# Kernel tuning notes

Hardware: AMD Instinct MI355X
Metric: run time of the kernel (lower is better)

## Reference

```python
import jax, jax.numpy as jnp
import numpy as np

HID = 64   # basis_hidden_dim
NB = 8     # num_learnable_bases
N = 16     # n_super_nodes
D = 4      # latent_dim
B = 2048   # batch

_PNAMES = ["W1", "b1", "W2", "b2", "W3", "b3", "scale", "aW1", "ab1", "aW2", "ab2", "res"]


def _basis_params(key, din):
    ks = jax.random.split(key, 4)
    s = 0.1
    return [
        jax.random.normal(ks[0], (NB, din, HID)) * s, jnp.zeros((NB, HID)),
        jax.random.normal(ks[1], (NB, HID, HID)) * s, jnp.zeros((NB, HID)),
        jax.random.normal(ks[2], (NB, HID, 1)) * s, jnp.zeros((NB, 1)),
        jnp.ones((NB,)),
        jax.random.normal(ks[3], (din, HID // 2)) * s, jnp.zeros((HID // 2,)),
        jax.random.normal(jax.random.fold_in(ks[3], 1), (HID // 2, NB)) * s, jnp.zeros((NB,)),
        jnp.ones((1,)) * 0.1,
    ]


def setup_inputs() -> dict:
    key = jax.random.key(0)
    k0, k1, k2, k3, k4 = jax.random.split(key, 5)
    inp = {"z_flat": jax.random.normal(k0, (B, N * D), dtype=jnp.float32)}
    for pfx, kk, din in [("pw", k1, 8), ("nd", k2, D), ("gl", k3, N * D)]:
        for nm, v in zip(_PNAMES, _basis_params(kk, din)):
            inp[pfx + "_" + nm] = v
    ks = jax.random.split(k4, 3)
    inp["sel_W1"] = jax.random.normal(ks[0], (N * D, HID)) * 0.1
    inp["sel_b1"] = jnp.zeros((HID,))
    inp["sel_W2"] = jax.random.normal(ks[1], (HID, HID // 2)) * 0.1
    inp["sel_b2"] = jnp.zeros((HID // 2,))
    inp["sel_W3"] = jax.random.normal(ks[2], (HID // 2, 1)) * 0.1
    inp["sel_b3"] = jnp.zeros((1,))
    return inp


def _basis(x, W1, b1, W2, b2, W3, b3, scale, aW1, ab1, aW2, ab2, res):
    # x: [..., din] -> [..., 1]. NB tiny 3-layer MLPs batched over basis axis n.
    h = jax.nn.silu(jnp.einsum('...i,nih->...nh', x, W1) + b1)
    h = jax.nn.silu(jnp.einsum('...nh,nhk->...nk', h, W2) + b2)
    o = (jnp.einsum('...nh,nh->...n', h, W3[..., 0]) + b3[:, 0]) * scale  # [..., NB]
    # attention mixing over the NB basis outputs
    a = jax.nn.silu(x @ aW1 + ab1)
    a = jax.nn.softmax(a @ aW2 + ab2, axis=-1)                            # [..., NB]
    out = jnp.sum(o * a, axis=-1, keepdims=True)
    return out + res * jnp.mean(x, axis=-1, keepdims=True)                # residual


def _forward(z_flat,
             pw_W1, pw_b1, pw_W2, pw_b2, pw_W3, pw_b3, pw_scale, pw_aW1, pw_ab1, pw_aW2, pw_ab2, pw_res,
             nd_W1, nd_b1, nd_W2, nd_b2, nd_W3, nd_b3, nd_scale, nd_aW1, nd_ab1, nd_aW2, nd_ab2, nd_res,
             gl_W1, gl_b1, gl_W2, gl_b2, gl_W3, gl_b3, gl_scale, gl_aW1, gl_ab1, gl_aW2, gl_ab2, gl_res,
             sel_W1, sel_b1, sel_W2, sel_b2, sel_W3, sel_b3):
    b = z_flat.shape[0]
    z_nodes = z_flat.reshape(b, N, D)
    pos = z_nodes[:, :, :2]
    iu, ju = jnp.triu_indices(N, k=1)  # P = N*(N-1)/2 = 120 pairs
    # pairwise distances on upper-triangular pairs (no box wrap: box_size=None)
    diffs = pos[:, iu] - pos[:, ju]                     # [B, P, 2]
    d = jnp.sqrt(jnp.sum(diffs * diffs, axis=-1))       # [B, P]
    d = jnp.maximum(d, 0.001)
    inv_d = 1.0 / (d + 0.1)
    inv_sq = 1.0 / (d * d + 0.1)
    exp_d = jnp.exp(-jnp.minimum(d, 20.0))
    screened = exp_d / (d + 0.1)
    log_d = jnp.log(d + 1.0)
    # learnable pairwise basis: cat(pos_i, vel_i, pos_j, vel_j) == cat(z_i, z_j) for D=4
    pair_in = jnp.concatenate([z_nodes[:, iu], z_nodes[:, ju]], axis=-1)  # [B, P, 8]
    pw = _basis(pair_in, pw_W1, pw_b1, pw_W2, pw_b2, pw_W3, pw_b3, pw_scale,
                pw_aW1, pw_ab1, pw_aW2, pw_ab2, pw_res)[..., 0]           # [B, P]
    nd = _basis(z_nodes, nd_W1, nd_b1, nd_W2, nd_b2, nd_W3, nd_b3, nd_scale,
                nd_aW1, nd_ab1, nd_aW2, nd_ab2, nd_res)[..., 0]           # [B, N]
    gl = _basis(z_flat, gl_W1, gl_b1, gl_W2, gl_b2, gl_W3, gl_b3, gl_scale,
                gl_aW1, gl_ab1, gl_aW2, gl_ab2, gl_res)                   # [B, 1]
    X = jnp.concatenate([z_flat, d, inv_d, inv_sq, exp_d, screened, log_d, pw, nd, gl], axis=1)
    # adaptive feature selection gate
    s = jax.nn.silu(z_flat @ sel_W1 + sel_b1)
    s = jax.nn.silu(s @ sel_W2 + sel_b2)
    s = jax.nn.sigmoid(s @ sel_W3 + sel_b3)             # [B, 1]
    X = X * s
    return jnp.clip(X, -1e6, 1e6)


def reference(z_flat,
              pw_W1, pw_b1, pw_W2, pw_b2, pw_W3, pw_b3, pw_scale, pw_aW1, pw_ab1, pw_aW2, pw_ab2, pw_res,
              nd_W1, nd_b1, nd_W2, nd_b2, nd_W3, nd_b3, nd_scale, nd_aW1, nd_ab1, nd_aW2, nd_ab2, nd_res,
              gl_W1, gl_b1, gl_W2, gl_b2, gl_W3, gl_b3, gl_scale, gl_aW1, gl_ab1, gl_aW2, gl_ab2, gl_res,
              sel_W1, sel_b1, sel_W2, sel_b2, sel_W3, sel_b3):
    return _forward(z_flat,
                    pw_W1, pw_b1, pw_W2, pw_b2, pw_W3, pw_b3, pw_scale, pw_aW1, pw_ab1, pw_aW2, pw_ab2, pw_res,
                    nd_W1, nd_b1, nd_W2, nd_b2, nd_W3, nd_b3, nd_scale, nd_aW1, nd_ab1, nd_aW2, nd_ab2, nd_res,
                    gl_W1, gl_b1, gl_W2, gl_b2, gl_W3, gl_b3, gl_scale, gl_aW1, gl_ab1, gl_aW2, gl_ab2, gl_res,
                    sel_W1, sel_b1, sel_W2, sel_b2, sel_W3, sel_b3)
```

## Files before the change

### kernel.cpp

```cpp
#include <hip/hip_runtime.h>
#include <hip/hip_bf16.h>
#include <math.h>

#define XCOLS 921
#define COL_Z 0
#define COL_D 64
#define COL_INVD 184
#define COL_INVSQ 304
#define COL_EXPD 424
#define COL_SCR 544
#define COL_LOGD 664
#define COL_PW 784
#define COL_ND 904
#define COL_GL 920

#define BATCH 2048
#define NPAIRS 120
#define RPW (BATCH * NPAIRS)
#define RND (BATCH * 16)
#define RGL BATCH
#define RTOT (RPW + RND + RGL)

#define PW_BLK 3840
#define ND_BLK 512
#define GL_BLK 32

#define WS_SGATE   0u
#define WS_ZERO    8192u
#define WS_B1D_PW  8448u
#define WS_B1D_ND  10496u
#define WS_B1D_GL  12544u
#define WS_BW3_PW  14592u
#define WS_BW3_ND  18688u
#define WS_BW3_GL  22784u
#define WS_W1T_PW  26880u
#define WS_W1T_ND  35072u
#define WS_W1T_GL  43264u
#define WS_W2T_PW  108800u
#define WS_W2T_ND  174336u
#define WS_W2T_GL  239872u
#define WS_XF      305408u
#define WS_XGL     4761856u
#define WS_ATT     5024000u
#define WS_TAIL    14002432u

typedef unsigned short ushort_t;
typedef unsigned int uint_t;
typedef __attribute__((ext_vector_type(8))) short bf16x8;
typedef __attribute__((ext_vector_type(4))) float f32x4;

__device__ __forceinline__ float fast_rcp(float x) { return __builtin_amdgcn_rcpf(x); }
__device__ __forceinline__ float silu_f(float x) { return x * fast_rcp(1.0f + __expf(-x)); }
__device__ __forceinline__ ushort_t f2b(float f) {
    __hip_bfloat16 h = __float2bfloat16(f);
    return __builtin_bit_cast(ushort_t, h);
}
__device__ __forceinline__ uint_t pk2(float a, float b) {
    return (uint_t)f2b(a) | ((uint_t)f2b(b) << 16);
}
__device__ __forceinline__ int permS(int m) {
    return ((m >> 2) & 3) * 8 + (m & 3) + ((m >> 4) & 1) * 4 + ((m >> 5) & 1) * 32;
}

struct AArgs { const float *aW1, *ab1, *aW2, *ab2, *b3, *scale, *res; };
struct PArgs { const float *W1, *b1, *W2, *b2, *W3; };

__global__ __launch_bounds__(64) void selgeom_kernel(
    const float* __restrict__ z,
    const float* __restrict__ W1, const float* __restrict__ b1,
    const float* __restrict__ W2, const float* __restrict__ b2,
    const float* __restrict__ W3, const float* __restrict__ b3,
    float* __restrict__ s_out, float* __restrict__ out)
{
    int b = blockIdx.x;
    int t = threadIdx.x;
    __shared__ float zs[64];
    __shared__ float h1[64];
    __shared__ float h2[32];
    __shared__ float sg;
    zs[t] = z[b * 64 + t];
    __syncthreads();
    {
        float acc = b1[t];
        #pragma unroll
        for (int i = 0; i < 64; ++i) acc += zs[i] * W1[i * 64 + t];
        h1[t] = silu_f(acc);
    }
    __syncthreads();
    if (t < 32) {
        float acc = b2[t];
        #pragma unroll
        for (int i = 0; i < 64; ++i) acc += h1[i] * W2[i * 32 + t];
        h2[t] = silu_f(acc);
    }
    __syncthreads();
    if (t == 0) {
        float acc = b3[0];
        #pragma unroll
        for (int i = 0; i < 32; ++i) acc += h2[i] * W3[i];
        float s = fast_rcp(1.0f + __expf(-acc));
        sg = s;
        s_out[b] = s;
    }
    __syncthreads();
    float s = sg;
    float* row = out + (size_t)b * XCOLS;
    {
        float v = zs[t] * s;
        row[COL_Z + t] = fminf(fmaxf(v, -1e6f), 1e6f);
    }
    #pragma unroll
    for (int rep = 0; rep < 2; ++rep) {
        int p = t + rep * 64;
        if (p < NPAIRS) {
            int i = 0, pp = p;
            while (pp >= 15 - i) { pp -= 15 - i; ++i; }
            int j = i + 1 + pp;
            float dx = zs[i * 4 + 0] - zs[j * 4 + 0];
            float dy = zs[i * 4 + 1] - zs[j * 4 + 1];
            float d = sqrtf(dx * dx + dy * dy);
            d = fmaxf(d, 0.001f);
            float inv_d = fast_rcp(d + 0.1f);
            float inv_sq = fast_rcp(d * d + 0.1f);
            float exp_d = __expf(-fminf(d, 20.0f));
            float screened = exp_d * inv_d;
            float log_d = __logf(d + 1.0f);
            row[COL_D + p] = d * s;
            row[COL_INVD + p] = inv_d * s;
            row[COL_INVSQ + p] = inv_sq * s;
            row[COL_EXPD + p] = exp_d * s;
            row[COL_SCR + p] = screened * s;
            row[COL_LOGD + p] = log_d * s;
        }
    }
}

__global__ __launch_bounds__(256) void xprep_kernel(
    const float* __restrict__ z,
    AArgs apw, AArgs anda, AArgs agl,
    PArgs ppw, PArgs pnd, PArgs pgl,
    char* __restrict__ ws)
{
    const int bid = blockIdx.x;
    if (bid >= 1096) {
        int t0 = (bid - 1096) * 256 + threadIdx.x;
        const int STR = 128 * 256;
        if (t0 < 64) ((float*)(ws + WS_ZERO))[t0] = 0.f;
        for (int t = t0; t < 8192; t += STR) {
            int u = t & 4095;
            int n = u >> 9, m = (u >> 3) & 63, k = u & 7;
            int sm = permS(m);
            if (t < 4096)
                ((ushort_t*)(ws + WS_W1T_PW))[u] = f2b(ppw.W1[n * 512 + k * 64 + sm]);
            else
                ((ushort_t*)(ws + WS_W1T_ND))[u] =
                    (k < 4) ? f2b(pnd.W1[n * 256 + k * 64 + sm]) : (ushort_t)0;
        }
        for (int t = t0; t < 32768; t += STR) {
            int n = t >> 12, m = (t >> 6) & 63, k = t & 63;
            ((ushort_t*)(ws + WS_W1T_GL))[t] = f2b(pgl.W1[n * 4096 + k * 64 + permS(m)]);
        }
        for (int t = t0; t < 3 * 32768; t += STR) {
            int which = t >> 15, u = t & 32767;
            int n = u >> 12, kb = (u >> 9) & 7, col = (u >> 3) & 63, e = u & 7;
            int k = (kb & 3) * 8 + e + ((kb >> 2) << 5);
            const float* src = which == 0 ? ppw.W2 : which == 1 ? pnd.W2 : pgl.W2;
            ushort_t* dst = (ushort_t*)(ws + (which == 0 ? WS_W2T_PW : which == 1 ? WS_W2T_ND : WS_W2T_GL));
            dst[u] = f2b(src[n * 4096 + k * 64 + col]);
        }
        for (int t = t0; t < 1536; t += STR) {
            int which = t >> 9, u = t & 511;
            int n = u >> 6, m = u & 63;
            const float* b1 = which == 0 ? ppw.b1 : which == 1 ? pnd.b1 : pgl.b1;
            float* dst = (float*)(ws + (which == 0 ? WS_B1D_PW : which == 1 ? WS_B1D_ND : WS_B1D_GL));
            dst[u] = b1[n * 64 + permS(m)];
        }
        for (int t = t0; t < 1536; t += STR) {
            int which = t >> 9, u = t & 511;
            const float* b2 = which == 0 ? ppw.b2 : which == 1 ? pnd.b2 : pgl.b2;
            const float* W3 = which == 0 ? ppw.W3 : which == 1 ? pnd.W3 : pgl.W3;
            float2* dst = (float2*)(ws + (which == 0 ? WS_BW3_PW : which == 1 ? WS_BW3_ND : WS_BW3_GL));
            dst[u] = make_float2(b2[u], W3[u]);
        }
        return;
    }

    const int urow = bid * 256 + threadIdx.x;
    const float* sg = (const float*)(ws + WS_SGATE);
    float a1acc[32];
    float mean, s;
    AArgs A;

    if (urow < RPW) {
        A = apw;
        int b = urow / 120, p = urow - b * 120;
        int i = 0, pp = p;
        while (pp >= 15 - i) { pp -= 15 - i; ++i; }
        int j = i + 1 + pp;
        const float* zb = z + b * 64;
        float4 xa = *(const float4*)(zb + i * 4);
        float4 xb = *(const float4*)(zb + j * 4);
        float x[8] = {xa.x, xa.y, xa.z, xa.w, xb.x, xb.y, xb.z, xb.w};
        uint4 xw = make_uint4(pk2(x[0], x[1]), pk2(x[2], x[3]), pk2(x[4], x[5]), pk2(x[6], x[7]));
        *(uint4*)(ws + WS_XF + (size_t)urow * 16) = xw;
        mean = (x[0] + x[1] + x[2] + x[3] + x[4] + x[5] + x[6] + x[7]) * 0.125f;
        #pragma unroll
        for (int u = 0; u < 32; ++u) {
            float acc = A.ab1[u];
            #pragma unroll
            for (int q = 0; q < 8; ++q) acc += x[q] * A.aW1[q * 32 + u];
            a1acc[u] = acc;
        }
        s = sg[b];
    } else if (urow < RPW + RND) {
        A = anda;
        int loc = urow - RPW;
        int b = loc >> 4, node = loc & 15;
        float4 xa = *(const float4*)(z + b * 64 + node * 4);
        float x[4] = {xa.x, xa.y, xa.z, xa.w};
        uint4 xw = make_uint4(pk2(x[0], x[1]), pk2(x[2], x[3]), 0u, 0u);
        *(uint4*)(ws + WS_XF + (size_t)urow * 16) = xw;
        mean = (x[0] + x[1] + x[2] + x[3]) * 0.25f;
        #pragma unroll
        for (int u = 0; u < 32; ++u) {
            float acc = A.ab1[u];
            #pragma unroll
            for (int q = 0; q < 4; ++q) acc += x[q] * A.aW1[q * 32 + u];
            a1acc[u] = acc;
        }
        s = sg[b];
    } else {
        A = agl;
        int r = urow - (RPW + RND);
        const float* zr = z + (size_t)r * 64;
        #pragma unroll
        for (int u = 0; u < 32; ++u) a1acc[u] = A.ab1[u];
        float mn = 0.f;
        #pragma unroll
        for (int c = 0; c < 8; ++c) {
            float4 f0 = *(const float4*)(zr + c * 8);
            float4 f1 = *(const float4*)(zr + c * 8 + 4);
            float xs[8] = {f0.x, f0.y, f0.z, f0.w, f1.x, f1.y, f1.z, f1.w};
            uint4 xw = make_uint4(pk2(xs[0], xs[1]), pk2(xs[2], xs[3]),
                                  pk2(xs[4], xs[5]), pk2(xs[6], xs[7]));
            *(uint4*)(ws + WS_XGL + (size_t)r * 128 + c * 16) = xw;
            #pragma unroll
            for (int q = 0; q < 8; ++q) {
                mn += xs[q];
                float xk = xs[q];
                #pragma unroll
                for (int u = 0; u < 32; ++u) a1acc[u] += xk * A.aW1[(c * 8 + q) * 32 + u];
            }
        }
        mean = mn * (1.0f / 64.0f);
        s = sg[r];
    }

    float lg[8];
    #pragma unroll
    for (int n = 0; n < 8; ++n) lg[n] = A.ab2[n];
    #pragma unroll
    for (int u = 0; u < 32; ++u) {
        float a1 = silu_f(a1acc[u]);
        #pragma unroll
        for (int n = 0; n < 8; ++n) lg[n] += a1 * A.aW2[u * 8 + n];
    }
    float m = lg[0];
    #pragma unroll
    for (int n = 1; n < 8; ++n) m = fmaxf(m, lg[n]);
    float sum = 0.f;
    #pragma unroll
    for (int n = 0; n < 8; ++n) { lg[n] = __expf(lg[n] - m); sum += lg[n]; }
    float inv = fast_rcp(sum);
    float tail = 0.f;
    float as_[8];
    #pragma unroll
    for (int n = 0; n < 8; ++n) {
        float a_n = lg[n] * inv * A.scale[n];
        tail += a_n * A.b3[n];
        as_[n] = a_n * s;
    }
    float* ag = (float*)(ws + WS_ATT) + (size_t)urow * 8;
    *(float4*)(ag + 0) = make_float4(as_[0], as_[1], as_[2], as_[3]);
    *(float4*)(ag + 4) = make_float4(as_[4], as_[5], as_[6], as_[7]);
    ((float*)(ws + WS_TAIL))[urow] = (tail + A.res[0] * mean) * s;
}

#define H2_EPILOGUE \
  { \
    const float* bp = b1base + n * 64 + g * 4; \
    float4 bb0 = *(const float4*)(bp); \
    float4 bb1 = *(const float4*)(bp + 16); \
    float4 bb2 = *(const float4*)(bp + 32); \
    float4 bb3 = *(const float4*)(bp + 48); \
    union { bf16x8 v; uint_t u[4]; } A0, A1; \
    A0.u[0] = pk2(silu_f(d0[0] + bb0.x), silu_f(d0[1] + bb0.y)); \
    A0.u[1] = pk2(silu_f(d0[2] + bb0.z), silu_f(d0[3] + bb0.w)); \
    A0.u[2] = pk2(silu_f(d1[0] + bb1.x), silu_f(d1[1] + bb1.y)); \
    A0.u[3] = pk2(silu_f(d1[2] + bb1.z), silu_f(d1[3] + bb1.w)); \
    A1.u[0] = pk2(silu_f(d2[0] + bb2.x), silu_f(d2[1] + bb2.y)); \
    A1.u[1] = pk2(silu_f(d2[2] + bb2.z), silu_f(d2[3] + bb2.w)); \
    A1.u[2] = pk2(silu_f(d3[0] + bb3.x), silu_f(d3[1] + bb3.y)); \
    A1.u[3] = pk2(silu_f(d3[2] + bb3.z), silu_f(d3[3] + bb3.w)); \
    const char* w2p = ws + (w2l + (uint_t)n * 8192u); \
    float pv0 = 0.f, pv1 = 0.f, pv2 = 0.f, pv3 = 0.f; \
    _Pragma("unroll") \
    for (int cb = 0; cb < 4; ++cb) { \
      bf16x8 bf0 = *(const bf16x8*)(w2p + cb * 256); \
      bf16x8 bf1 = *(const bf16x8*)(w2p + cb * 256 + 4096); \
      f32x4 acc = {0.f, 0.f, 0.f, 0.f}; \
      acc = __builtin_amdgcn_mfma_f32_16x16x32_bf16(A0.v, bf0, acc, 0, 0, 0); \
      acc = __builtin_amdgcn_mfma_f32_16x16x32_bf16(A1.v, bf1, acc, 0, 0, 0); \
      float2 bw = bwbase[n * 64 + cb * 16 + lo]; \
      pv0 += silu_f(acc[0] + bw.x) * bw.y; \
      pv1 += silu_f(acc[1] + bw.x) * bw.y; \
      pv2 += silu_f(acc[2] + bw.x) * bw.y; \
      pv3 += silu_f(acc[3] + bw.x) * bw.y; \
    } \
    oa0 += Att[attb + 0 * 9 + n] * pv0; \
    oa1 += Att[attb + 1 * 9 + n] * pv1; \
    oa2 += Att[attb + 2 * 9 + n] * pv2; \
    oa3 += Att[attb + 3 * 9 + n] * pv3; \
  }

__global__ __launch_bounds__(256, 4) void basis_main_kernel(
    const char* __restrict__ ws, float* __restrict__ out)
{
    __shared__ float Att[64 * 9];
    const int tid = threadIdx.x;
    const int lane = tid & 63;
    const int wave = tid >> 6;
    const int g = lane >> 4;
    const int lo = lane & 15;

    const int bid = blockIdx.x;
    int fam, rowbase, ubase;
    uint_t w1t_off, w2t_off, b1d_off, bw3_off;
    if (bid < GL_BLK) {
        fam = 2; rowbase = bid * 64; ubase = RPW + RND + rowbase;
        w1t_off = WS_W1T_GL; w2t_off = WS_W2T_GL; b1d_off = WS_B1D_GL; bw3_off = WS_BW3_GL;
    } else if (bid < GL_BLK + PW_BLK) {
        fam = 0; rowbase = (bid - GL_BLK) * 64; ubase = rowbase;
        w1t_off = WS_W1T_PW; w2t_off = WS_W2T_PW; b1d_off = WS_B1D_PW; bw3_off = WS_BW3_PW;
    } else {
        fam = 1; rowbase = (bid - (GL_BLK + PW_BLK)) * 64; ubase = RPW + rowbase;
        w1t_off = WS_W1T_ND; w2t_off = WS_W2T_ND; b1d_off = WS_B1D_ND; bw3_off = WS_BW3_ND;
    }

    {
        const float* ag = (const float*)(ws + WS_ATT) + (size_t)ubase * 8;
        #pragma unroll
        for (int q = 0; q < 2; ++q) {
            int idx = tid + q * 256;
            Att[(idx >> 3) * 9 + (idx & 7)] = ag[idx];
        }
        if (tid < 64) Att[tid * 9 + 8] = ((const float*)(ws + WS_TAIL))[ubase + tid];
    }

    bf16x8 xf0, xf1;
    if (fam == 2) {
        const char* xg = ws + WS_XGL + (size_t)(rowbase + wave * 16 + lo) * 128;
        xf0 = *(const bf16x8*)(xg + g * 16);
        xf1 = *(const bf16x8*)(xg + 64 + g * 16);
    } else {
        uint_t xoff = (g == 0) ? (WS_XF + (uint_t)(ubase + wave * 16 + lo) * 16u) : WS_ZERO;
        xf0 = *(const bf16x8*)(ws + xoff);
    }
    __syncthreads();

    const float* b1base = (const float*)(ws + b1d_off);
    const float2* bwbase = (const float2*)(ws + bw3_off);
    const int attb = (wave * 16 + g * 4) * 9;
    const uint_t w2l = w2t_off + (uint_t)(g * 1024 + lo * 16);

    float oa0 = 0.f, oa1 = 0.f, oa2 = 0.f, oa3 = 0.f;
    const f32x4 zr4 = {0.f, 0.f, 0.f, 0.f};

    if (fam != 2) {
        const uint_t abase = w1t_off + (uint_t)(lo * 16);
        for (int n = 0; n < 8; ++n) {
            uint_t an = abase + (uint_t)n * 1024u;
            bf16x8 af0 = *(const bf16x8*)(ws + ((g == 0) ? an : WS_ZERO));
            bf16x8 af1 = *(const bf16x8*)(ws + ((g == 0) ? an + 256u : WS_ZERO));
            bf16x8 af2 = *(const bf16x8*)(ws + ((g == 0) ? an + 512u : WS_ZERO));
            bf16x8 af3 = *(const bf16x8*)(ws + ((g == 0) ? an + 768u : WS_ZERO));
            f32x4 d0 = __builtin_amdgcn_mfma_f32_16x16x32_bf16(af0, xf0, zr4, 0, 0, 0);
            f32x4 d1 = __builtin_amdgcn_mfma_f32_16x16x32_bf16(af1, xf0, zr4, 0, 0, 0);
            f32x4 d2 = __builtin_amdgcn_mfma_f32_16x16x32_bf16(af2, xf0, zr4, 0, 0, 0);
            f32x4 d3 = __builtin_amdgcn_mfma_f32_16x16x32_bf16(af3, xf0, zr4, 0, 0, 0);
            H2_EPILOGUE
        }
    } else {
        const uint_t abase = w1t_off + (uint_t)(lo * 128 + g * 16);
        for (int n = 0; n < 8; ++n) {
            const char* w1n = ws + (abase + (uint_t)n * 8192u);
            f32x4 d0 = __builtin_amdgcn_mfma_f32_16x16x32_bf16(*(const bf16x8*)(w1n +    0), xf0, zr4, 0, 0, 0);
            d0 = __builtin_amdgcn_mfma_f32_16x16x32_bf16(*(const bf16x8*)(w1n +   64), xf1, d0, 0, 0, 0);
            f32x4 d1 = __builtin_amdgcn_mfma_f32_16x16x32_bf16(*(const bf16x8*)(w1n + 2048), xf0, zr4, 0, 0, 0);
            d1 = __builtin_amdgcn_mfma_f32_16x16x32_bf16(*(const bf16x8*)(w1n + 2112), xf1, d1, 0, 0, 0);
            f32x4 d2 = __builtin_amdgcn_mfma_f32_16x16x32_bf16(*(const bf16x8*)(w1n + 4096), xf0, zr4, 0, 0, 0);
            d2 = __builtin_amdgcn_mfma_f32_16x16x32_bf16(*(const bf16x8*)(w1n + 4160), xf1, d2, 0, 0, 0);
            f32x4 d3 = __builtin_amdgcn_mfma_f32_16x16x32_bf16(*(const bf16x8*)(w1n + 6144), xf0, zr4, 0, 0, 0);
            d3 = __builtin_amdgcn_mfma_f32_16x16x32_bf16(*(const bf16x8*)(w1n + 6208), xf1, d3, 0, 0, 0);
            H2_EPILOGUE
        }
    }

    float ov[4] = {oa0, oa1, oa2, oa3};
    #pragma unroll
    for (int r = 0; r < 4; ++r) {
        float v = ov[r];
        v += __shfl_xor(v, 1);
        v += __shfl_xor(v, 2);
        v += __shfl_xor(v, 4);
        v += __shfl_xor(v, 8);
        if (lo == 0) {
            int row_l = wave * 16 + g * 4 + r;
            int rg = rowbase + row_l;
            int bb, colo;
            if (fam == 0) { bb = rg / 120; colo = COL_PW + (rg - bb * 120); }
            else if (fam == 1) { bb = rg >> 4; colo = COL_ND + (rg & 15); }
            else { bb = rg; colo = COL_GL; }
            float o = v + Att[row_l * 9 + 8];
            o = fminf(fmaxf(o, -1e6f), 1e6f);
            out[(size_t)bb * XCOLS + colo] = o;
        }
    }
}

extern "C" void kernel_launch(void* const* d_in, const int* in_sizes, int n_in,
                              void* d_out, int out_size, void* d_ws, size_t ws_size,
                              hipStream_t stream) {
    const float* z = (const float*)d_in[0];
    const float* pw[12]; const float* nd[12]; const float* gl[12];
    for (int i = 0; i < 12; ++i) pw[i] = (const float*)d_in[1 + i];
    for (int i = 0; i < 12; ++i) nd[i] = (const float*)d_in[13 + i];
    for (int i = 0; i < 12; ++i) gl[i] = (const float*)d_in[25 + i];
    const float* sel_W1 = (const float*)d_in[37];
    const float* sel_b1 = (const float*)d_in[38];
    const float* sel_W2 = (const float*)d_in[39];
    const float* sel_b2 = (const float*)d_in[40];
    const float* sel_W3 = (const float*)d_in[41];
    const float* sel_b3 = (const float*)d_in[42];

    float* out = (float*)d_out;
    char* ws = (char*)d_ws;

    selgeom_kernel<<<BATCH, 64, 0, stream>>>(
        z, sel_W1, sel_b1, sel_W2, sel_b2, sel_W3, sel_b3,
        (float*)(ws + WS_SGATE), out);

    AArgs apw = {pw[7], pw[8], pw[9], pw[10], pw[5], pw[6], pw[11]};
    AArgs anda = {nd[7], nd[8], nd[9], nd[10], nd[5], nd[6], nd[11]};
    AArgs agl = {gl[7], gl[8], gl[9], gl[10], gl[5], gl[6], gl[11]};
    PArgs ppw = {pw[0], pw[1], pw[2], pw[3], pw[4]};
    PArgs pnd = {nd[0], nd[1], nd[2], nd[3], nd[4]};
    PArgs pgl = {gl[0], gl[1], gl[2], gl[3], gl[4]};

    xprep_kernel<<<1096 + 128, 256, 0, stream>>>(z, apw, anda, agl, ppw, pnd, pgl, ws);

    basis_main_kernel<<<GL_BLK + PW_BLK + ND_BLK, 256, 0, stream>>>(ws, out);
}
```

Before: 137.1 us.

## Assign one basis per wave and keep its weights in registers across row tiles

The main kernel now uses 512-thread blocks that cover 128 rows, with each of the 8 waves owning one basis MLP. Each wave loads its W1/W2 fragments and bias/W3 pairs into registers once, then loops over 8 row tiles, instead of reloading weights for every basis on every block. For the pairwise and node families the layer-1 bias is folded into the MFMA through a constant-one input lane. Per-basis partial sums go to shared memory and are reduced after a barrier, which adds register pressure and an extra synchronisation.

```diff
diff --git a/kernel.cpp b/kernel.cpp
--- a/kernel.cpp
+++ b/kernel.cpp
@@ -21,28 +21,29 @@
 #define RGL BATCH
 #define RTOT (RPW + RND + RGL)
 
-#define PW_BLK 3840
-#define ND_BLK 512
-#define GL_BLK 32
+#define ROWS_BLK 128
+#define TILES 8
+#define GL_BLK 16
+#define PW_BLK 1920
+#define ND_BLK 256
 
 #define WS_SGATE   0u
 #define WS_ZERO    8192u
-#define WS_B1D_PW  8448u
-#define WS_B1D_ND  10496u
-#define WS_B1D_GL  12544u
-#define WS_BW3_PW  14592u
-#define WS_BW3_ND  18688u
-#define WS_BW3_GL  22784u
-#define WS_W1T_PW  26880u
-#define WS_W1T_ND  35072u
-#define WS_W1T_GL  43264u
-#define WS_W2T_PW  108800u
-#define WS_W2T_ND  174336u
-#define WS_W2T_GL  239872u
-#define WS_XF      305408u
-#define WS_XGL     4761856u
-#define WS_ATT     5024000u
-#define WS_TAIL    14002432u
+#define WS_ONE     8448u
+#define WS_BW3_PW  8704u
+#define WS_BW3_ND  12800u
+#define WS_BW3_GL  16896u
+#define WS_B1D_GL  20992u
+#define WS_W1T_PW  23040u
+#define WS_W1T_ND  39424u
+#define WS_W1T_GL  55808u
+#define WS_W2T_PW  121344u
+#define WS_W2T_ND  186880u
+#define WS_W2T_GL  252416u
+#define WS_XF      317952u
+#define WS_XGL     4774400u
+#define WS_ATT     5036544u
+#define WS_TAIL    14014976u
 
 typedef unsigned short ushort_t;
 typedef unsigned int uint_t;
@@ -146,34 +147,35 @@
         int t0 = (bid - 1096) * 256 + threadIdx.x;
         const int STR = 128 * 256;
         if (t0 < 64) ((float*)(ws + WS_ZERO))[t0] = 0.f;
-        for (int t = t0; t < 8192; t += STR) {
-            int u = t & 4095;
-            int n = u >> 9, m = (u >> 3) & 63, k = u & 7;
+        if (t0 < 8) ((ushort_t*)(ws + WS_ONE))[t0] = (t0 == 0) ? f2b(1.0f) : (ushort_t)0;
+        for (int t = t0; t < 16384; t += STR) {
+            int which = t >> 13, u = t & 8191;
+            int nn = u >> 10, m = (u >> 4) & 63, k = u & 15;
             int sm = permS(m);
-            if (t < 4096)
-                ((ushort_t*)(ws + WS_W1T_PW))[u] = f2b(ppw.W1[n * 512 + k * 64 + sm]);
+            float v;
+            if (which == 0)
+                v = (k < 8) ? ppw.W1[nn * 512 + k * 64 + sm]
+                  : (k == 8 ? ppw.b1[nn * 64 + sm] : 0.f);
             else
-                ((ushort_t*)(ws + WS_W1T_ND))[u] =
-                    (k < 4) ? f2b(pnd.W1[n * 256 + k * 64 + sm]) : (ushort_t)0;
+                v = (k < 4) ? pnd.W1[nn * 256 + k * 64 + sm]
+                  : (k == 8 ? pnd.b1[nn * 64 + sm] : 0.f);
+            ((ushort_t*)(ws + (which == 0 ? WS_W1T_PW : WS_W1T_ND)))[u] = f2b(v);
         }
         for (int t = t0; t < 32768; t += STR) {
-            int n = t >> 12, m = (t >> 6) & 63, k = t & 63;
-            ((ushort_t*)(ws + WS_W1T_GL))[t] = f2b(pgl.W1[n * 4096 + k * 64 + permS(m)]);
+            int nn = t >> 12, m = (t >> 6) & 63, k = t & 63;
+            ((ushort_t*)(ws + WS_W1T_GL))[t] = f2b(pgl.W1[nn * 4096 + k * 64 + permS(m)]);
+        }
+        for (int t = t0; t < 512; t += STR) {
+            int nn = t >> 6, m = t & 63;
+            ((float*)(ws + WS_B1D_GL))[t] = pgl.b1[nn * 64 + permS(m)];
         }
         for (int t = t0; t < 3 * 32768; t += STR) {
             int which = t >> 15, u = t & 32767;
-            int n = u >> 12, kb = (u >> 9) & 7, col = (u >> 3) & 63, e = u & 7;
+            int nn = u >> 12, kb = (u >> 9) & 7, col = (u >> 3) & 63, e = u & 7;
             int k = (kb & 3) * 8 + e + ((kb >> 2) << 5);
             const float* src = which == 0 ? ppw.W2 : which == 1 ? pnd.W2 : pgl.W2;
             ushort_t* dst = (ushort_t*)(ws + (which == 0 ? WS_W2T_PW : which == 1 ? WS_W2T_ND : WS_W2T_GL));
-            dst[u] = f2b(src[n * 4096 + k * 64 + col]);
-        }
-        for (int t = t0; t < 1536; t += STR) {
-            int which = t >> 9, u = t & 511;
-            int n = u >> 6, m = u & 63;
-            const float* b1 = which == 0 ? ppw.b1 : which == 1 ? pnd.b1 : pgl.b1;
-            float* dst = (float*)(ws + (which == 0 ? WS_B1D_PW : which == 1 ? WS_B1D_ND : WS_B1D_GL));
-            dst[u] = b1[n * 64 + permS(m)];
+            dst[u] = f2b(src[nn * 4096 + k * 64 + col]);
         }
         for (int t = t0; t < 1536; t += STR) {
             int which = t >> 9, u = t & 511;
@@ -286,145 +288,174 @@
     ((float*)(ws + WS_TAIL))[urow] = (tail + A.res[0] * mean) * s;
 }
 
-#define H2_EPILOGUE \
-  { \
-    const float* bp = b1base + n * 64 + g * 4; \
-    float4 bb0 = *(const float4*)(bp); \
-    float4 bb1 = *(const float4*)(bp + 16); \
-    float4 bb2 = *(const float4*)(bp + 32); \
-    float4 bb3 = *(const float4*)(bp + 48); \
-    union { bf16x8 v; uint_t u[4]; } A0, A1; \
-    A0.u[0] = pk2(silu_f(d0[0] + bb0.x), silu_f(d0[1] + bb0.y)); \
-    A0.u[1] = pk2(silu_f(d0[2] + bb0.z), silu_f(d0[3] + bb0.w)); \
-    A0.u[2] = pk2(silu_f(d1[0] + bb1.x), silu_f(d1[1] + bb1.y)); \
-    A0.u[3] = pk2(silu_f(d1[2] + bb1.z), silu_f(d1[3] + bb1.w)); \
-    A1.u[0] = pk2(silu_f(d2[0] + bb2.x), silu_f(d2[1] + bb2.y)); \
-    A1.u[1] = pk2(silu_f(d2[2] + bb2.z), silu_f(d2[3] + bb2.w)); \
-    A1.u[2] = pk2(silu_f(d3[0] + bb3.x), silu_f(d3[1] + bb3.y)); \
-    A1.u[3] = pk2(silu_f(d3[2] + bb3.z), silu_f(d3[3] + bb3.w)); \
-    const char* w2p = ws + (w2l + (uint_t)n * 8192u); \
-    float pv0 = 0.f, pv1 = 0.f, pv2 = 0.f, pv3 = 0.f; \
-    _Pragma("unroll") \
-    for (int cb = 0; cb < 4; ++cb) { \
-      bf16x8 bf0 = *(const bf16x8*)(w2p + cb * 256); \
-      bf16x8 bf1 = *(const bf16x8*)(w2p + cb * 256 + 4096); \
-      f32x4 acc = {0.f, 0.f, 0.f, 0.f}; \
-      acc = __builtin_amdgcn_mfma_f32_16x16x32_bf16(A0.v, bf0, acc, 0, 0, 0); \
-      acc = __builtin_amdgcn_mfma_f32_16x16x32_bf16(A1.v, bf1, acc, 0, 0, 0); \
-      float2 bw = bwbase[n * 64 + cb * 16 + lo]; \
-      pv0 += silu_f(acc[0] + bw.x) * bw.y; \
-      pv1 += silu_f(acc[1] + bw.x) * bw.y; \
-      pv2 += silu_f(acc[2] + bw.x) * bw.y; \
-      pv3 += silu_f(acc[3] + bw.x) * bw.y; \
-    } \
-    oa0 += Att[attb + 0 * 9 + n] * pv0; \
-    oa1 += Att[attb + 1 * 9 + n] * pv1; \
-    oa2 += Att[attb + 2 * 9 + n] * pv2; \
-    oa3 += Att[attb + 3 * 9 + n] * pv3; \
-  }
-
-__global__ __launch_bounds__(256, 4) void basis_main_kernel(
+__global__ __launch_bounds__(512, 4) void basis_main_kernel(
     const char* __restrict__ ws, float* __restrict__ out)
 {
-    __shared__ float Att[64 * 9];
+    __shared__ float Att[ROWS_BLK * 9];
+    __shared__ float Part[8][ROWS_BLK];
     const int tid = threadIdx.x;
     const int lane = tid & 63;
-    const int wave = tid >> 6;
+    const int n = tid >> 6;
     const int g = lane >> 4;
     const int lo = lane & 15;
 
     const int bid = blockIdx.x;
     int fam, rowbase, ubase;
-    uint_t w1t_off, w2t_off, b1d_off, bw3_off;
+    uint_t w1t_off, w2t_off, bw3_off;
     if (bid < GL_BLK) {
-        fam = 2; rowbase = bid * 64; ubase = RPW + RND + rowbase;
-        w1t_off = WS_W1T_GL; w2t_off = WS_W2T_GL; b1d_off = WS_B1D_GL; bw3_off = WS_BW3_GL;
+        fam = 2; rowbase = bid * ROWS_BLK; ubase = RPW + RND + rowbase;
+        w1t_off = WS_W1T_GL; w2t_off = WS_W2T_GL; bw3_off = WS_BW3_GL;
     } else if (bid < GL_BLK + PW_BLK) {
-        fam = 0; rowbase = (bid - GL_BLK) * 64; ubase = rowbase;
-        w1t_off = WS_W1T_PW; w2t_off = WS_W2T_PW; b1d_off = WS_B1D_PW; bw3_off = WS_BW3_PW;
+        fam = 0; rowbase = (bid - GL_BLK) * ROWS_BLK; ubase = rowbase;
+        w1t_off = WS_W1T_PW; w2t_off = WS_W2T_PW; bw3_off = WS_BW3_PW;
     } else {
-        fam = 1; rowbase = (bid - (GL_BLK + PW_BLK)) * 64; ubase = RPW + rowbase;
-        w1t_off = WS_W1T_ND; w2t_off = WS_W2T_ND; b1d_off = WS_B1D_ND; bw3_off = WS_BW3_ND;
+        fam = 1; rowbase = (bid - (GL_BLK + PW_BLK)) * ROWS_BLK; ubase = RPW + rowbase;
+        w1t_off = WS_W1T_ND; w2t_off = WS_W2T_ND; bw3_off = WS_BW3_ND;
     }
 
     {
         const float* ag = (const float*)(ws + WS_ATT) + (size_t)ubase * 8;
         #pragma unroll
         for (int q = 0; q < 2; ++q) {
-            int idx = tid + q * 256;
+            int idx = tid + q * 512;
             Att[(idx >> 3) * 9 + (idx & 7)] = ag[idx];
         }
-        if (tid < 64) Att[tid * 9 + 8] = ((const float*)(ws + WS_TAIL))[ubase + tid];
-    }
-
-    bf16x8 xf0, xf1;
-    if (fam == 2) {
-        const char* xg = ws + WS_XGL + (size_t)(rowbase + wave * 16 + lo) * 128;
-        xf0 = *(const bf16x8*)(xg + g * 16);
-        xf1 = *(const bf16x8*)(xg + 64 + g * 16);
+        if (tid < ROWS_BLK) Att[tid * 9 + 8] = ((const float*)(ws + WS_TAIL))[ubase + tid];
+    }
+
+    const char* w2base = ws + w2t_off + (uint_t)(n * 8192 + g * 1024 + lo * 16);
+    bf16x8 w2f0[4], w2f1[4];
+    #pragma unroll
+    for (int cb = 0; cb < 4; ++cb) {
+        w2f0[cb] = *(const bf16x8*)(w2base + cb * 256);
+        w2f1[cb] = *(const bf16x8*)(w2base + cb * 256 + 4096);
+    }
+    float2 bw[4];
+    #pragma unroll
+    for (int cb = 0; cb < 4; ++cb)
+        bw[cb] = ((const float2*)(ws + bw3_off))[n * 64 + cb * 16 + lo];
+
+    __syncthreads();
+
+    const f32x4 zr4 = {0.f, 0.f, 0.f, 0.f};
+
+    if (fam != 2) {
+        bf16x8 af[4];
+        #pragma unroll
+        for (int mt = 0; mt < 4; ++mt) {
+            uint_t a = (g < 2) ? (w1t_off + (uint_t)(n * 2048 + (mt * 16 + lo) * 32 + g * 16))
+                               : WS_ZERO;
+            af[mt] = *(const bf16x8*)(ws + a);
+        }
+        #pragma unroll 1
+        for (int t = 0; t < TILES; ++t) {
+            uint_t xoff = (g == 0) ? (WS_XF + (uint_t)(ubase + t * 16 + lo) * 16u)
+                        : (g == 1) ? WS_ONE : WS_ZERO;
+            bf16x8 xf = *(const bf16x8*)(ws + xoff);
+            f32x4 d0 = __builtin_amdgcn_mfma_f32_16x16x32_bf16(af[0], xf, zr4, 0, 0, 0);
+            f32x4 d1 = __builtin_amdgcn_mfma_f32_16x16x32_bf16(af[1], xf, zr4, 0, 0, 0);
+            f32x4 d2 = __builtin_amdgcn_mfma_f32_16x16x32_bf16(af[2], xf, zr4, 0, 0, 0);
+            f32x4 d3 = __builtin_amdgcn_mfma_f32_16x16x32_bf16(af[3], xf, zr4, 0, 0, 0);
+            union { bf16x8 v; uint_t u[4]; } A0, A1;
+            A0.u[0] = pk2(silu_f(d0[0]), silu_f(d0[1]));
+            A0.u[1] = pk2(silu_f(d0[2]), silu_f(d0[3]));
+            A0.u[2] = pk2(silu_f(d1[0]), silu_f(d1[1]));
+            A0.u[3] = pk2(silu_f(d1[2]), silu_f(d1[3]));
+            A1.u[0] = pk2(silu_f(d2[0]), silu_f(d2[1]));
+            A1.u[1] = pk2(silu_f(d2[2]), silu_f(d2[3]));
+            A1.u[2] = pk2(silu_f(d3[0]), silu_f(d3[1]));
+            A1.u[3] = pk2(silu_f(d3[2]), silu_f(d3[3]));
+            float pv0 = 0.f, pv1 = 0.f, pv2 = 0.f, pv3 = 0.f;
+            #pragma unroll
+            for (int cb = 0; cb < 4; ++cb) {
+                f32x4 acc = __builtin_amdgcn_mfma_f32_16x16x32_bf16(A0.v, w2f0[cb], zr4, 0, 0, 0);
+                acc = __builtin_amdgcn_mfma_f32_16x16x32_bf16(A1.v, w2f1[cb], acc, 0, 0, 0);
+                pv0 += silu_f(acc[0] + bw[cb].x) * bw[cb].y;
+                pv1 += silu_f(acc[1] + bw[cb].x) * bw[cb].y;
+                pv2 += silu_f(acc[2] + bw[cb].x) * bw[cb].y;
+                pv3 += silu_f(acc[3] + bw[cb].x) * bw[cb].y;
+            }
+            float pvv[4] = {pv0, pv1, pv2, pv3};
+            #pragma unroll
+            for (int r = 0; r < 4; ++r) {
+                float v = pvv[r];
+                v += __shfl_xor(v, 1);
+                v += __shfl_xor(v, 2);
+                v += __shfl_xor(v, 4);
+                v += __shfl_xor(v, 8);
+                if (lo == 0) {
+                    int row = t * 16 + g * 4 + r;
+                    Part[n][row] = Att[row * 9 + n] * v;
+                }
+            }
+        }
     } else {
-        uint_t xoff = (g == 0) ? (WS_XF + (uint_t)(ubase + wave * 16 + lo) * 16u) : WS_ZERO;
-        xf0 = *(const bf16x8*)(ws + xoff);
-    }
-    __syncthreads();
-
-    const float* b1base = (const float*)(ws + b1d_off);
-    const float2* bwbase = (const float2*)(ws + bw3_off);
-    const int attb = (wave * 16 + g * 4) * 9;
-    const uint_t w2l = w2t_off + (uint_t)(g * 1024 + lo * 16);
-
-    float oa0 = 0.f, oa1 = 0.f, oa2 = 0.f, oa3 = 0.f;
-    const f32x4 zr4 = {0.f, 0.f, 0.f, 0.f};
-
-    if (fam != 2) {
-        const uint_t abase = w1t_off + (uint_t)(lo * 16);
-        for (int n = 0; n < 8; ++n) {
-            uint_t an = abase + (uint_t)n * 1024u;
-            bf16x8 af0 = *(const bf16x8*)(ws + ((g == 0) ? an : WS_ZERO));
-            bf16x8 af1 = *(const bf16x8*)(ws + ((g == 0) ? an + 256u : WS_ZERO));
-            bf16x8 af2 = *(const bf16x8*)(ws + ((g == 0) ? an + 512u : WS_ZERO));
-            bf16x8 af3 = *(const bf16x8*)(ws + ((g == 0) ? an + 768u : WS_ZERO));
-            f32x4 d0 = __builtin_amdgcn_mfma_f32_16x16x32_bf16(af0, xf0, zr4, 0, 0, 0);
-            f32x4 d1 = __builtin_amdgcn_mfma_f32_16x16x32_bf16(af1, xf0, zr4, 0, 0, 0);
-            f32x4 d2 = __builtin_amdgcn_mfma_f32_16x16x32_bf16(af2, xf0, zr4, 0, 0, 0);
-            f32x4 d3 = __builtin_amdgcn_mfma_f32_16x16x32_bf16(af3, xf0, zr4, 0, 0, 0);
-            H2_EPILOGUE
-        }
-    } else {
-        const uint_t abase = w1t_off + (uint_t)(lo * 128 + g * 16);
-        for (int n = 0; n < 8; ++n) {
-            const char* w1n = ws + (abase + (uint_t)n * 8192u);
-            f32x4 d0 = __builtin_amdgcn_mfma_f32_16x16x32_bf16(*(const bf16x8*)(w1n +    0), xf0, zr4, 0, 0, 0);
-            d0 = __builtin_amdgcn_mfma_f32_16x16x32_bf16(*(const bf16x8*)(w1n +   64), xf1, d0, 0, 0, 0);
-            f32x4 d1 = __builtin_amdgcn_mfma_f32_16x16x32_bf16(*(const bf16x8*)(w1n + 2048), xf0, zr4, 0, 0, 0);
-            d1 = __builtin_amdgcn_mfma_f32_16x16x32_bf16(*(const bf16x8*)(w1n + 2112), xf1, d1, 0, 0, 0);
-            f32x4 d2 = __builtin_amdgcn_mfma_f32_16x16x32_bf16(*(const bf16x8*)(w1n + 4096), xf0, zr4, 0, 0, 0);
-            d2 = __builtin_amdgcn_mfma_f32_16x16x32_bf16(*(const bf16x8*)(w1n + 4160), xf1, d2, 0, 0, 0);
-            f32x4 d3 = __builtin_amdgcn_mfma_f32_16x16x32_bf16(*(const bf16x8*)(w1n + 6144), xf0, zr4, 0, 0, 0);
-            d3 = __builtin_amdgcn_mfma_f32_16x16x32_bf16(*(const bf16x8*)(w1n + 6208), xf1, d3, 0, 0, 0);
-            H2_EPILOGUE
-        }
-    }
-
-    float ov[4] = {oa0, oa1, oa2, oa3};
-    #pragma unroll
-    for (int r = 0; r < 4; ++r) {
-        float v = ov[r];
-        v += __shfl_xor(v, 1);
-        v += __shfl_xor(v, 2);
-        v += __shfl_xor(v, 4);
-        v += __shfl_xor(v, 8);
-        if (lo == 0) {
-            int row_l = wave * 16 + g * 4 + r;
-            int rg = rowbase + row_l;
-            int bb, colo;
-            if (fam == 0) { bb = rg / 120; colo = COL_PW + (rg - bb * 120); }
-            else if (fam == 1) { bb = rg >> 4; colo = COL_ND + (rg & 15); }
-            else { bb = rg; colo = COL_GL; }
-            float o = v + Att[row_l * 9 + 8];
-            o = fminf(fmaxf(o, -1e6f), 1e6f);
-            out[(size_t)bb * XCOLS + colo] = o;
-        }
+        float4 b1r[4];
+        #pragma unroll
+        for (int mt = 0; mt < 4; ++mt)
+            b1r[mt] = *(const float4*)(ws + WS_B1D_GL + (uint_t)(n * 64 + mt * 16 + g * 4) * 4u);
+        const char* w1b = ws + w1t_off + (uint_t)(n * 8192 + g * 16 + lo * 128);
+        #pragma unroll 1
+        for (int t = 0; t < TILES; ++t) {
+            const char* xg = ws + WS_XGL + (size_t)(rowbase + t * 16 + lo) * 128;
+            bf16x8 xf0 = *(const bf16x8*)(xg + g * 16);
+            bf16x8 xf1 = *(const bf16x8*)(xg + 64 + g * 16);
+            f32x4 d0 = __builtin_amdgcn_mfma_f32_16x16x32_bf16(*(const bf16x8*)(w1b + 0), xf0, zr4, 0, 0, 0);
+            d0 = __builtin_amdgcn_mfma_f32_16x16x32_bf16(*(const bf16x8*)(w1b + 64), xf1, d0, 0, 0, 0);
+            f32x4 d1 = __builtin_amdgcn_mfma_f32_16x16x32_bf16(*(const bf16x8*)(w1b + 2048), xf0, zr4, 0, 0, 0);
+            d1 = __builtin_amdgcn_mfma_f32_16x16x32_bf16(*(const bf16x8*)(w1b + 2112), xf1, d1, 0, 0, 0);
+            f32x4 d2 = __builtin_amdgcn_mfma_f32_16x16x32_bf16(*(const bf16x8*)(w1b + 4096), xf0, zr4, 0, 0, 0);
+            d2 = __builtin_amdgcn_mfma_f32_16x16x32_bf16(*(const bf16x8*)(w1b + 4160), xf1, d2, 0, 0, 0);
+            f32x4 d3 = __builtin_amdgcn_mfma_f32_16x16x32_bf16(*(const bf16x8*)(w1b + 6144), xf0, zr4, 0, 0, 0);
+            d3 = __builtin_amdgcn_mfma_f32_16x16x32_bf16(*(const bf16x8*)(w1b + 6208), xf1, d3, 0, 0, 0);
+            union { bf16x8 v; uint_t u[4]; } A0, A1;
+            A0.u[0] = pk2(silu_f(d0[0] + b1r[0].x), silu_f(d0[1] + b1r[0].y));
+            A0.u[1] = pk2(silu_f(d0[2] + b1r[0].z), silu_f(d0[3] + b1r[0].w));
+            A0.u[2] = pk2(silu_f(d1[0] + b1r[1].x), silu_f(d1[1] + b1r[1].y));
+            A0.u[3] = pk2(silu_f(d1[2] + b1r[1].z), silu_f(d1[3] + b1r[1].w));
+            A1.u[0] = pk2(silu_f(d2[0] + b1r[2].x), silu_f(d2[1] + b1r[2].y));
+            A1.u[1] = pk2(silu_f(d2[2] + b1r[2].z), silu_f(d2[3] + b1r[2].w));
+            A1.u[2] = pk2(silu_f(d3[0] + b1r[3].x), silu_f(d3[1] + b1r[3].y));
+            A1.u[3] = pk2(silu_f(d3[2] + b1r[3].z), silu_f(d3[3] + b1r[3].w));
+            float pv0 = 0.f, pv1 = 0.f, pv2 = 0.f, pv3 = 0.f;
+            #pragma unroll
+            for (int cb = 0; cb < 4; ++cb) {
+                f32x4 acc = __builtin_amdgcn_mfma_f32_16x16x32_bf16(A0.v, w2f0[cb], zr4, 0, 0, 0);
+                acc = __builtin_amdgcn_mfma_f32_16x16x32_bf16(A1.v, w2f1[cb], acc, 0, 0, 0);
+                pv0 += silu_f(acc[0] + bw[cb].x) * bw[cb].y;
+                pv1 += silu_f(acc[1] + bw[cb].x) * bw[cb].y;
+                pv2 += silu_f(acc[2] + bw[cb].x) * bw[cb].y;
+                pv3 += silu_f(acc[3] + bw[cb].x) * bw[cb].y;
+            }
+            float pvv[4] = {pv0, pv1, pv2, pv3};
+            #pragma unroll
+            for (int r = 0; r < 4; ++r) {
+                float v = pvv[r];
+                v += __shfl_xor(v, 1);
+                v += __shfl_xor(v, 2);
+                v += __shfl_xor(v, 4);
+                v += __shfl_xor(v, 8);
+                if (lo == 0) {
+                    int row = t * 16 + g * 4 + r;
+                    Part[n][row] = Att[row * 9 + n] * v;
+                }
+            }
+        }
+    }
+
+    __syncthreads();
+
+    if (tid < ROWS_BLK) {
+        float v = Att[tid * 9 + 8];
+        #pragma unroll
+        for (int w = 0; w < 8; ++w) v += Part[w][tid];
+        v = fminf(fmaxf(v, -1e6f), 1e6f);
+        int rg = rowbase + tid;
+        int bb, colo;
+        if (fam == 0) { bb = rg / 120; colo = COL_PW + (rg - bb * 120); }
+        else if (fam == 1) { bb = rg >> 4; colo = COL_ND + (rg & 15); }
+        else { bb = rg; colo = COL_GL; }
+        out[(size_t)bb * XCOLS + colo] = v;
     }
 }
 
@@ -459,5 +490,5 @@
 
     xprep_kernel<<<1096 + 128, 256, 0, stream>>>(z, apw, anda, agl, ppw, pnd, pgl, ws);
 
-    basis_main_kernel<<<GL_BLK + PW_BLK + ND_BLK, 256, 0, stream>>>(ws, out);
-}
+    basis_main_kernel<<<GL_BLK + PW_BLK + ND_BLK, 512, 0, stream>>>(ws, out);
+}
```

Result: faster. 128.0 us (-6.7%).
